# Kernel optimization log

Measured on AMD Instinct MI355X. Metric: run time of the kernel, lower is better.

Reference implementation:

```python
import jax, jax.numpy as jnp
import numpy as np
import math

DIM = 1024
NUM_HEADS = 16
HEAD_DIM = 64
NUM_FEATURES = 128
B, N = 2, 1024


def _sample_orf(rng, num_features, head_dim):
    # Orthogonal Random Features: stack QR-orthogonalized blocks scaled by chi(D) row norms
    blocks = []
    while len(blocks) * head_dim < num_features:
        G = rng.standard_normal((head_dim, head_dim)).astype(np.float32)
        Q, _ = np.linalg.qr(G)
        norms = np.linalg.norm(rng.standard_normal((head_dim, head_dim)).astype(np.float32), axis=1)
        blocks.append(np.diag(norms) @ Q.T)
    return np.concatenate(blocks, axis=0)[:num_features]


def setup_inputs() -> dict:
    key = jax.random.key(0)
    ks = jax.random.split(key, 6)
    s = 1.0 / math.sqrt(DIM)
    x = jax.random.normal(ks[0], (B, N, DIM), dtype=jnp.float32)
    omega = jnp.asarray(_sample_orf(np.random.default_rng(0), NUM_FEATURES, HEAD_DIM))
    Wq = jax.random.normal(ks[1], (DIM, DIM), dtype=jnp.float32) * s
    Wk = jax.random.normal(ks[2], (DIM, DIM), dtype=jnp.float32) * s
    Wv = jax.random.normal(ks[3], (DIM, DIM), dtype=jnp.float32) * s
    Wo = jax.random.normal(ks[4], (DIM, DIM), dtype=jnp.float32) * s
    bo = jax.random.normal(ks[5], (DIM,), dtype=jnp.float32) * 0.01
    return {"x": x, "omega": omega, "Wq": Wq, "Wk": Wk, "Wv": Wv, "Wo": Wo, "bo": bo}


def _phi(x, omega, is_query):
    # x: [B,H,N,D], omega: [M,D] -> [B,H,N,M]
    proj = jnp.einsum('bhnd,md->bhnm', x, omega)
    norm = 0.5 * jnp.sum(x * x, axis=-1, keepdims=True)
    log_phi = proj - norm
    if is_query:
        log_phi = log_phi - jnp.max(log_phi, axis=-1, keepdims=True)
    else:
        log_phi = log_phi - jnp.max(log_phi)
    return jnp.exp(log_phi) / math.sqrt(NUM_FEATURES) + 1e-4


def reference(x, omega, Wq, Wk, Wv, Wo, bo):
    Bx, Nx, _ = x.shape
    H, D = NUM_HEADS, HEAD_DIM

    def split_heads(y):  # [B,N,H*D] -> [B,H,N,D]
        return y.reshape(Bx, Nx, H, D).transpose(0, 2, 1, 3)

    q = split_heads(x @ Wq.T)
    k = split_heads(x @ Wk.T)
    v = split_heads(x @ Wv.T)

    scale = D ** (-0.25)
    phi_q = _phi(q * scale, omega, is_query=True)   # [B,H,N,M]
    phi_k = _phi(k * scale, omega, is_query=False)  # [B,H,N,M]

    # causal linear attention via explicit kv outer-product cumsum (as in source)
    kv = jnp.einsum('bhnm,bhnd->bhnmd', phi_k, v)
    kv_cumsum = jnp.cumsum(kv, axis=2)              # [B,H,N,M,D]
    k_cumsum = jnp.cumsum(phi_k, axis=2)            # [B,H,N,M]
    out = jnp.einsum('bhnm,bhnmd->bhnd', phi_q, kv_cumsum)
    z = 1.0 / (jnp.einsum('bhnm,bhnm->bhn', phi_q, k_cumsum) + 1e-6)
    out = out * z[..., None]

    out = out.transpose(0, 2, 1, 3).reshape(Bx, Nx, H * D)
    return out @ Wo.T + bo
```

## Files before the change

### kernel.cpp

```cpp
#include <hip/hip_runtime.h>
#include <hip/hip_bf16.h>
#include <math.h>

#define DIMS 1024
#define NHEADS 16
#define HDIM 64
#define NFEAT 128
#define BB 2
#define NN 1024
#define BN (BB*NN)
#define NCH 16
#define CSZ 64
#define WW (DIMS*DIMS)
#define QKVN (3*DIMS)

#define SCALE 0.3535533905932738f
#define INV_SQRT_M 0.08838834764831845f

typedef __attribute__((ext_vector_type(8))) _Float16 h8v;
typedef __attribute__((ext_vector_type(8))) short s8v;
typedef __attribute__((ext_vector_type(4))) float f4v;

__device__ __forceinline__ ushort f2h(float x) {
    _Float16 h = (_Float16)x;
    return *(ushort*)&h;
}
__device__ __forceinline__ float h2f(ushort u) {
    _Float16 h = *(_Float16*)&u;
    return (float)h;
}
__device__ __forceinline__ void gload16(const void* g, void* l) {
    __builtin_amdgcn_global_load_lds(
        (const __attribute__((address_space(1))) unsigned int*)g,
        (__attribute__((address_space(3))) unsigned int*)l,
        16, 0, 0);
}

#define NX (BN*DIMS/8)
#define NW (WW/8)
#define NOM (NFEAT*HDIM/8)
__global__ __launch_bounds__(256) void cast_all(const float* __restrict__ x,
                                                const float* __restrict__ Wq,
                                                const float* __restrict__ Wk,
                                                const float* __restrict__ Wv,
                                                const float* __restrict__ Wo,
                                                const float* __restrict__ omega,
                                                ushort* __restrict__ xh,
                                                ushort* __restrict__ wqkvh,
                                                ushort* __restrict__ woh,
                                                ushort* __restrict__ omh) {
    const int i = blockIdx.x * 256 + threadIdx.x;
    const float* src; ushort* dst; int off;
    if (i < NX)               { src = x;     dst = xh;                     off = i; }
    else if (i < NX + NW)     { src = Wq;    dst = wqkvh;                  off = i - NX; }
    else if (i < NX + 2 * NW) { src = Wk;    dst = wqkvh + WW;             off = i - NX - NW; }
    else if (i < NX + 3 * NW) { src = Wv;    dst = wqkvh + 2 * (size_t)WW; off = i - NX - 2 * NW; }
    else if (i < NX + 4 * NW) { src = Wo;    dst = woh;                    off = i - NX - 3 * NW; }
    else                      { src = omega; dst = omh;                    off = i - NX - 4 * NW; }
    float4 a = ((const float4*)src)[2 * (size_t)off];
    float4 b = ((const float4*)src)[2 * (size_t)off + 1];
    float v[8] = {a.x, a.y, a.z, a.w, b.x, b.y, b.z, b.w};
    ushort h8[8];
    #pragma unroll
    for (int j = 0; j < 8; ++j) h8[j] = f2h(v[j]);
    *(s8v*)&dst[(size_t)off * 8] = *(s8v*)&h8[0];
}

template<int BM, bool HOUT>
__global__ __launch_bounds__(256) void gemm_nt_lds(const ushort* __restrict__ A,
                                                   const ushort* __restrict__ B,
                                                   float* __restrict__ C,
                                                   ushort* __restrict__ C16,
                                                   const float* __restrict__ bias,
                                                   int M, int N, int K, int nbx) {
    constexpr int MF = BM / 32;
    constexpr int AI = BM / 32;
    __shared__ __attribute__((aligned(16))) ushort lA[BM][64];
    __shared__ __attribute__((aligned(16))) ushort lB[128][64];
    const int tid = threadIdx.x;
    const int w = tid >> 6, l = tid & 63, lr = l & 15, lg = l >> 4;
    const int wm = (w >> 1) * (BM / 2), wn = (w & 1) * 64;
    const int nwg = gridDim.x;
    const int q8 = nwg >> 3;
    const int neu = (blockIdx.x & 7) * q8 + (blockIdx.x >> 3);
    const int bx = neu % nbx, by = neu / nbx;
    const int bi = bx * BM, bj = by * 128;
    const int srow = l >> 3;
    const int scol = ((l & 7) ^ (l >> 3)) * 8;

    f4v acc[MF][4] = {};
    for (int k0 = 0; k0 < K; k0 += 64) {
        #pragma unroll
        for (int i = 0; i < AI; ++i) {
            const int r0 = w * (8 * AI) + i * 8;
            gload16(&A[(size_t)(bi + r0 + srow) * K + k0 + scol], &lA[r0][0]);
        }
        #pragma unroll
        for (int i = 0; i < 4; ++i) {
            const int r0 = w * 32 + i * 8;
            gload16(&B[(size_t)(bj + r0 + srow) * K + k0 + scol], &lB[r0][0]);
        }
        __syncthreads();
        #pragma unroll
        for (int kk = 0; kk < 2; ++kk) {
            const int soff = ((kk * 4 + lg) ^ (lr & 7)) * 8;
            h8v b_[4];
            #pragma unroll
            for (int j = 0; j < 4; ++j) b_[j] = *(h8v*)&lB[wn + j * 16 + lr][soff];
            #pragma unroll
            for (int i = 0; i < MF; ++i) {
                h8v a_ = *(h8v*)&lA[wm + i * 16 + lr][soff];
                #pragma unroll
                for (int j = 0; j < 4; ++j)
                    acc[i][j] = __builtin_amdgcn_mfma_f32_16x16x32_f16(a_, b_[j], acc[i][j], 0, 0, 0);
            }
        }
        __syncthreads();
    }
    #pragma unroll
    for (int i = 0; i < MF; ++i)
        #pragma unroll
        for (int j = 0; j < 4; ++j)
            #pragma unroll
            for (int rg = 0; rg < 4; ++rg) {
                const int row = bi + wm + i * 16 + lg * 4 + rg;
                const int col = bj + wn + j * 16 + lr;
                if (HOUT) {
                    C16[(size_t)row * N + col] = f2h(acc[i][j][rg]);
                } else {
                    float r = acc[i][j][rg] + bias[col];
                    C[(size_t)row * N + col] = r;
                }
            }
}

__global__ __launch_bounds__(256) void phi_mfma(const ushort* __restrict__ qkvh,
                                                const ushort* __restrict__ omh,
                                                ushort* __restrict__ phiq,
                                                ushort* __restrict__ plocal,
                                                float* __restrict__ blockmax,
                                                ushort* __restrict__ vt,
                                                ushort* __restrict__ ssum16,
                                                float* __restrict__ kcsum,
                                                float* __restrict__ vsum) {
    __shared__ __attribute__((aligned(16))) ushort lq[64][72];
    __shared__ __attribute__((aligned(16))) ushort lom[128 * 72];
    __shared__ __attribute__((aligned(16))) ushort lktT[128][72];
    __shared__ __attribute__((aligned(16))) ushort lv[64][72];
    __shared__ __attribute__((aligned(16))) ushort lvt[64][72];
    __shared__ float lnorm[64];
    __shared__ float wred[4];
    const int tid = threadIdx.x;
    const int z = blockIdx.z, h = blockIdx.y;
    const int bn0 = blockIdx.x * 64;
    const int w = tid >> 6, l = tid & 63, lr = l & 15, lg = l >> 4;
    const int b = blockIdx.x >> 4, c = blockIdx.x & 15;
    const int bh = b * NHEADS + h;

    {
        const int r = tid >> 2, c0 = (tid & 3) * 16;
        const size_t g = (size_t)(bn0 + r) * QKVN + (size_t)z * DIMS + h * HDIM + c0;
        s8v v0 = *(const s8v*)&qkvh[g];
        s8v v1 = *(const s8v*)&qkvh[g + 8];
        *(s8v*)&lq[r][c0] = v0;
        *(s8v*)&lq[r][c0 + 8] = v1;
        float p = 0.f;
        #pragma unroll
        for (int j = 0; j < 8; ++j) {
            float a = h2f(((ushort*)&v0)[j]); p += a * a;
            float bb2 = h2f(((ushort*)&v1)[j]); p += bb2 * bb2;
        }
        p += __shfl_xor(p, 1); p += __shfl_xor(p, 2);
        if ((tid & 3) == 0) lnorm[r] = p;
    }
    {
        const int m = tid >> 1, c0 = (tid & 1) * 32;
        #pragma unroll
        for (int i = 0; i < 4; ++i)
            *(s8v*)&lom[m * 72 + c0 + i * 8] = *(const s8v*)&omh[m * HDIM + c0 + i * 8];
    }
    if (z == 1) {
        const int r = tid >> 2, c0 = (tid & 3) * 16;
        const size_t g = (size_t)(bn0 + r) * QKVN + 2 * DIMS + h * HDIM + c0;
        *(s8v*)&lv[r][c0]     = *(const s8v*)&qkvh[g];
        *(s8v*)&lv[r][c0 + 8] = *(const s8v*)&qkvh[g + 8];
    }
    __syncthreads();

    f4v acc[8] = {};
    #pragma unroll
    for (int k0 = 0; k0 < 64; k0 += 32) {
        h8v a = *(h8v*)&lq[w * 16 + lr][k0 + lg * 8];
        #pragma unroll
        for (int ct = 0; ct < 8; ++ct) {
            h8v bo = *(h8v*)&lom[(ct * 16 + lr) * 72 + k0 + lg * 8];
            acc[ct] = __builtin_amdgcn_mfma_f32_16x16x32_f16(a, bo, acc[ct], 0, 0, 0);
        }
    }

    const float hs2 = 0.5f * SCALE * SCALE;
    float lvv[4][8];
    #pragma unroll
    for (int rg = 0; rg < 4; ++rg) {
        const int row = w * 16 + lg * 4 + rg;
        const float nh = hs2 * lnorm[row];
        #pragma unroll
        for (int ct = 0; ct < 8; ++ct) lvv[rg][ct] = SCALE * acc[ct][rg] - nh;
    }
    if (z == 1) {
        float bmax = -3.4e38f;
        #pragma unroll
        for (int rg = 0; rg < 4; ++rg)
            #pragma unroll
            for (int ct = 0; ct < 8; ++ct) bmax = fmaxf(bmax, lvv[rg][ct]);
        #pragma unroll
        for (int o = 32; o >= 1; o >>= 1) bmax = fmaxf(bmax, __shfl_xor(bmax, o));
        if (l == 0) wred[w] = bmax;
    }
    __syncthreads();

    if (z == 0) {
        #pragma unroll
        for (int rg = 0; rg < 4; ++rg) {
            const int row = w * 16 + lg * 4 + rg;
            float mx = -3.4e38f;
            #pragma unroll
            for (int ct = 0; ct < 8; ++ct) mx = fmaxf(mx, lvv[rg][ct]);
            #pragma unroll
            for (int o = 8; o >= 1; o >>= 1) mx = fmaxf(mx, __shfl_xor(mx, o));
            #pragma unroll
            for (int ct = 0; ct < 8; ++ct)
                lom[row * 136 + ct * 16 + lr] = f2h(expf(lvv[rg][ct] - mx) * INV_SQRT_M + 1e-4f);
        }
    } else {
        const float bm = fmaxf(fmaxf(wred[0], wred[1]), fmaxf(wred[2], wred[3]));
        if (tid == 0) blockmax[h * 32 + blockIdx.x] = bm;
        #pragma unroll
        for (int rg = 0; rg < 4; ++rg) {
            const int row = w * 16 + lg * 4 + rg;
            #pragma unroll
            for (int ct = 0; ct < 8; ++ct)
                lom[row * 136 + ct * 16 + lr] = f2h(expf(lvv[rg][ct] - bm));
        }
    }
    __syncthreads();

    {
        ushort* dst = (z == 0) ? phiq : plocal;
        const int r = tid >> 2, c0 = (tid & 3) * 32;
        const int br = bn0 + r;
        const int bb2 = br >> 10, n = br & (NN - 1);
        const size_t og = ((size_t)(bb2 * NHEADS + h) * NN + n) * NFEAT;
        #pragma unroll
        for (int i = 0; i < 4; ++i)
            *(s8v*)&dst[og + c0 + i * 8] = *(s8v*)&lom[r * 136 + c0 + i * 8];
    }
    if (z == 0) return;

    {
        const int m = tid >> 1, nh2 = (tid & 1) * 32;
        ushort tp[32];
        #pragma unroll
        for (int i = 0; i < 32; ++i) tp[i] = lom[(nh2 + i) * 136 + m];
        #pragma unroll
        for (int i = 0; i < 4; ++i) *(s8v*)&lktT[m][nh2 + i * 8] = *(s8v*)&tp[i * 8];
    }
    {
        const int d = tid >> 2, s0 = (tid & 3) * 16;
        ushort tp[16];
        #pragma unroll
        for (int i = 0; i < 16; ++i) tp[i] = lv[s0 + i][d];
        const size_t tb = ((size_t)bh * HDIM + d) * NN + c * CSZ + s0;
        *(s8v*)&vt[tb] = *(s8v*)&tp[0];
        *(s8v*)&vt[tb + 8] = *(s8v*)&tp[8];
        *(s8v*)&lvt[d][s0] = *(s8v*)&tp[0];
        *(s8v*)&lvt[d][s0 + 8] = *(s8v*)&tp[8];
    }
    __syncthreads();

    f4v ac2[8] = {};
    #pragma unroll
    for (int k0 = 0; k0 < 64; k0 += 32) {
        h8v a = *(h8v*)&lvt[w * 16 + lr][k0 + lg * 8];
        #pragma unroll
        for (int ct = 0; ct < 8; ++ct) {
            h8v bf = *(h8v*)&lktT[ct * 16 + lr][k0 + lg * 8];
            ac2[ct] = __builtin_amdgcn_mfma_f32_16x16x32_f16(a, bf, ac2[ct], 0, 0, 0);
        }
    }
    const size_t obase = ((size_t)bh * NCH + c) * (HDIM * NFEAT);
    #pragma unroll
    for (int ct = 0; ct < 8; ++ct)
        #pragma unroll
        for (int rg = 0; rg < 4; ++rg) {
            const int d = w * 16 + lg * 4 + rg, m = ct * 16 + lr;
            ssum16[obase + (size_t)d * NFEAT + m] = f2h(ac2[ct][rg]);
        }
    if (tid < 128) {
        float s = 0.f;
        #pragma unroll 8
        for (int i = 0; i < 64; ++i) s += h2f(lktT[tid][i]);
        kcsum[((size_t)bh * NCH + c) * NFEAT + tid] = s;
    }
    if (tid < 64) {
        float s = 0.f;
        #pragma unroll 8
        for (int i = 0; i < 64; ++i) s += h2f(lvt[tid][i]);
        vsum[((size_t)bh * NCH + c) * HDIM + tid] = s;
    }
}

__global__ __launch_bounds__(256) void scan_final(const ushort* __restrict__ phiq,
                                                  const ushort* __restrict__ plocal,
                                                  const ushort* __restrict__ vt,
                                                  const ushort* __restrict__ ssum16,
                                                  const float* __restrict__ kcsum,
                                                  const float* __restrict__ vsum,
                                                  const float* __restrict__ blockmax,
                                                  ushort* __restrict__ att_h) {
    const int c = blockIdx.x, bh = blockIdx.y;
    const int b = bh >> 4, h = bh & 15;
    const int n0 = c * CSZ;
    __shared__ __attribute__((aligned(16))) ushort lq[64][136];
    __shared__ __attribute__((aligned(16))) ushort lk[64][136];
    __shared__ __attribute__((aligned(16))) ushort lvt[64][72];
    __shared__ __attribute__((aligned(16))) ushort lsp[64][136];
    __shared__ __attribute__((aligned(16))) ushort lA[64][72];
    __shared__ float kc[NFEAT];
    __shared__ float zin[64];
    __shared__ float zp[4][64];
    __shared__ float gred[4];
    const int tid = threadIdx.x;

    float mxv = fmaxf(blockmax[tid], blockmax[tid + 256]);
    #pragma unroll
    for (int o = 32; o >= 1; o >>= 1) mxv = fmaxf(mxv, __shfl_xor(mxv, o));
    if ((tid & 63) == 0) gred[tid >> 6] = mxv;
    __syncthreads();
    const float gm = fmaxf(fmaxf(gred[0], gred[1]), fmaxf(gred[2], gred[3]));
    const float fac = expf(blockmax[h * 32 + b * 16 + c] - gm) * INV_SQRT_M;

    const size_t qb = ((size_t)bh * NN + n0) * NFEAT;
    #pragma unroll
    for (int i = 0; i < 4; ++i) {
        const int idx = tid + 256 * i;
        const int r = idx >> 4, cs = (idx & 15) * 8;
        *(s8v*)&lq[r][cs] = *(const s8v*)&phiq[qb + (size_t)r * NFEAT + cs];
        s8v pv = *(const s8v*)&plocal[qb + (size_t)r * NFEAT + cs];
        ushort t[8];
        #pragma unroll
        for (int j = 0; j < 8; ++j) t[j] = f2h(h2f(((ushort*)&pv)[j]) * fac + 1e-4f);
        *(s8v*)&lk[r][cs] = *(s8v*)&t[0];
    }
    {
        const int d = tid >> 2;
        const int m0 = (tid & 3) * 32;
        float acc[32] = {};
        float vs_tot = 0.f;
        for (int cp = 0; cp < c; ++cp) {
            const float facp = expf(blockmax[h * 32 + b * 16 + cp] - gm) * INV_SQRT_M;
            vs_tot += vsum[((size_t)bh * NCH + cp) * HDIM + d];
            const size_t cb = ((size_t)bh * NCH + cp) * (HDIM * NFEAT) + (size_t)d * NFEAT + m0;
            #pragma unroll
            for (int i = 0; i < 4; ++i) {
                s8v v = *(const s8v*)&ssum16[cb + i * 8];
                #pragma unroll
                for (int j = 0; j < 8; ++j) acc[i * 8 + j] += facp * h2f(((ushort*)&v)[j]);
            }
        }
        const float vadd = 1e-4f * vs_tot;
        ushort o[32];
        #pragma unroll
        for (int i = 0; i < 32; ++i) o[i] = f2h(acc[i] + vadd);
        #pragma unroll
        for (int i = 0; i < 4; ++i) *(s8v*)&lsp[d][m0 + i * 8] = *(s8v*)&o[i * 8];
    }
    if (tid < NFEAT) {
        float a = 0.f;
        for (int cp = 0; cp < c; ++cp) {
            const float facp = expf(blockmax[h * 32 + b * 16 + cp] - gm) * INV_SQRT_M;
            a += facp * kcsum[((size_t)bh * NCH + cp) * NFEAT + tid] + 64.0f * 1e-4f;
        }
        kc[tid] = a;
    }
    {
        const int d = tid >> 2, s = (tid & 3) * 16;
        const size_t g = ((size_t)bh * HDIM + d) * NN + n0 + s;
        *(s8v*)&lvt[d][s]     = *(const s8v*)&vt[g];
        *(s8v*)&lvt[d][s + 8] = *(const s8v*)&vt[g + 8];
    }
    __syncthreads();

    const int w = tid >> 6, l = tid & 63, lr = l & 15, lg = l >> 4;

    f4v a4[4] = {};
    #pragma unroll
    for (int k0 = 0; k0 < 128; k0 += 32) {
        h8v av = *(h8v*)&lq[w * 16 + lr][k0 + lg * 8];
        #pragma unroll
        for (int ct = 0; ct < 4; ++ct) {
            h8v bv = *(h8v*)&lk[ct * 16 + lr][k0 + lg * 8];
            a4[ct] = __builtin_amdgcn_mfma_f32_16x16x32_f16(av, bv, a4[ct], 0, 0, 0);
        }
    }
    float zi[4] = {0.f, 0.f, 0.f, 0.f};
    #pragma unroll
    for (int ct = 0; ct < 4; ++ct) {
        #pragma unroll
        for (int rg = 0; rg < 4; ++rg) {
            const int row = w * 16 + lg * 4 + rg;
            const int col = ct * 16 + lr;
            const float val = (col <= row) ? a4[ct][rg] : 0.f;
            const ushort hq = f2h(val);
            zi[rg] += h2f(hq);
            lA[row][col] = hq;
        }
    }
    #pragma unroll
    for (int rg = 0; rg < 4; ++rg) {
        float z = zi[rg];
        z += __shfl_xor(z, 1); z += __shfl_xor(z, 2);
        z += __shfl_xor(z, 4); z += __shfl_xor(z, 8);
        if (lr == 0) zin[w * 16 + lg * 4 + rg] = z;
    }
    {
        const int row = tid & 63, qq = tid >> 6;
        float s = 0.f;
        #pragma unroll 8
        for (int m = 0; m < 32; ++m) s += h2f(lq[row][qq * 32 + m]) * kc[qq * 32 + m];
        zp[qq][row] = s;
    }
    __syncthreads();

    f4v o4[4] = {};
    #pragma unroll
    for (int k0 = 0; k0 < 64; k0 += 32) {
        h8v av = *(h8v*)&lA[w * 16 + lr][k0 + lg * 8];
        #pragma unroll
        for (int ct = 0; ct < 4; ++ct) {
            h8v bv = *(h8v*)&lvt[ct * 16 + lr][k0 + lg * 8];
            o4[ct] = __builtin_amdgcn_mfma_f32_16x16x32_f16(av, bv, o4[ct], 0, 0, 0);
        }
    }
    #pragma unroll
    for (int k0 = 0; k0 < 128; k0 += 32) {
        h8v av = *(h8v*)&lq[w * 16 + lr][k0 + lg * 8];
        #pragma unroll
        for (int ct = 0; ct < 4; ++ct) {
            h8v bv = *(h8v*)&lsp[ct * 16 + lr][k0 + lg * 8];
            o4[ct] = __builtin_amdgcn_mfma_f32_16x16x32_f16(av, bv, o4[ct], 0, 0, 0);
        }
    }
    #pragma unroll
    for (int rg = 0; rg < 4; ++rg) {
        const int row = w * 16 + lg * 4 + rg;
        const float z = zin[row] + zp[0][row] + zp[1][row] + zp[2][row] + zp[3][row] + 1e-6f;
        const float rz = 1.f / z;
        #pragma unroll
        for (int ct = 0; ct < 4; ++ct) {
            const int d = ct * 16 + lr;
            att_h[((size_t)(b * NN + n0 + row)) * DIMS + h * HDIM + d] = f2h(o4[ct][rg] * rz);
        }
    }
}

extern "C" void kernel_launch(void* const* d_in, const int* in_sizes, int n_in,
                              void* d_out, int out_size, void* d_ws, size_t ws_size,
                              hipStream_t stream) {
    const float* x     = (const float*)d_in[0];
    const float* omega = (const float*)d_in[1];
    const float* Wq    = (const float*)d_in[2];
    const float* Wk    = (const float*)d_in[3];
    const float* Wv    = (const float*)d_in[4];
    const float* Wo    = (const float*)d_in[5];
    const float* bo    = (const float*)d_in[6];
    float* out = (float*)d_out;

    const size_t PROJ = (size_t)BN * DIMS;
    const size_t PHI  = (size_t)BB * NHEADS * NN * NFEAT;
    ushort* qkvh    = (ushort*)d_ws;
    ushort* xh      = qkvh + (size_t)BN * QKVN;
    ushort* wqkvh   = xh + PROJ;
    ushort* woh     = wqkvh + (size_t)QKVN * DIMS;
    ushort* omh     = woh + WW;
    ushort* phiq_h  = omh + NFEAT * HDIM;
    ushort* plocal  = phiq_h + PHI;
    ushort* vt_h    = plocal + PHI;
    ushort* ssum16  = vt_h + PROJ;
    ushort* att_hb  = ssum16 + PHI;
    float*  kcsum   = (float*)(att_hb + PROJ);
    float*  blockmax= kcsum + 32 * NCH * NFEAT;
    float*  vsum    = blockmax + 512;

    cast_all<<<(NX + 4 * NW + NOM) / 256, 256, 0, stream>>>(x, Wq, Wk, Wv, Wo, omega,
                                                            xh, wqkvh, woh, omh);

    gemm_nt_lds<64, true><<<(BN / 64) * (QKVN / 128), 256, 0, stream>>>(
        xh, wqkvh, nullptr, qkvh, nullptr, BN, QKVN, DIMS, BN / 64);

    dim3 pg(BN / 64, NHEADS, 2);
    phi_mfma<<<pg, 256, 0, stream>>>(qkvh, omh, phiq_h, plocal, blockmax,
                                     vt_h, ssum16, kcsum, vsum);

    dim3 cg(NCH, BB * NHEADS);
    scan_final<<<cg, 256, 0, stream>>>(phiq_h, plocal, vt_h, ssum16, kcsum, vsum,
                                       blockmax, att_hb);

    gemm_nt_lds<64, false><<<(BN / 64) * (DIMS / 128), 256, 0, stream>>>(
        att_hb, woh, out, nullptr, bo, BN, DIMS, DIMS, BN / 64);
}
```

Measured before the change: 86.26 us.

## Recompute phi features inside scan kernel instead of materializing phi_q and phi_k

The phi kernel no longer computes or stores phi_q and the local phi_k tensors. It now only produces the key-side block max, the transposed V, and the per-chunk summaries. The scan kernel recomputes phi_q and phi_k from the fp16 q/k projections and omega with MFMA, using a shared-memory pool that aliases buffers across phases. This removes the 2x fp16 [B,H,N,M] write and read round trip and halves the phi grid, at the cost of repeated feature-projection MFMAs and extra barriers in the scan kernel. The output projection GEMM tile height also drops from 64 to 32 rows, which doubles its block count.

```diff
diff --git a/kernel.cpp b/kernel.cpp
--- a/kernel.cpp
+++ b/kernel.cpp
@@ -134,15 +134,13 @@
             }
 }
 
-__global__ __launch_bounds__(256) void phi_mfma(const ushort* __restrict__ qkvh,
-                                                const ushort* __restrict__ omh,
-                                                ushort* __restrict__ phiq,
-                                                ushort* __restrict__ plocal,
-                                                float* __restrict__ blockmax,
-                                                ushort* __restrict__ vt,
-                                                ushort* __restrict__ ssum16,
-                                                float* __restrict__ kcsum,
-                                                float* __restrict__ vsum) {
+__global__ __launch_bounds__(256) void phik_stats(const ushort* __restrict__ qkvh,
+                                                  const ushort* __restrict__ omh,
+                                                  float* __restrict__ blockmax,
+                                                  ushort* __restrict__ vt,
+                                                  ushort* __restrict__ ssum16,
+                                                  float* __restrict__ kcsum,
+                                                  float* __restrict__ vsum) {
     __shared__ __attribute__((aligned(16))) ushort lq[64][72];
     __shared__ __attribute__((aligned(16))) ushort lom[128 * 72];
     __shared__ __attribute__((aligned(16))) ushort lktT[128][72];
@@ -151,7 +149,7 @@
     __shared__ float lnorm[64];
     __shared__ float wred[4];
     const int tid = threadIdx.x;
-    const int z = blockIdx.z, h = blockIdx.y;
+    const int h = blockIdx.y;
     const int bn0 = blockIdx.x * 64;
     const int w = tid >> 6, l = tid & 63, lr = l & 15, lg = l >> 4;
     const int b = blockIdx.x >> 4, c = blockIdx.x & 15;
@@ -159,7 +157,7 @@
 
     {
         const int r = tid >> 2, c0 = (tid & 3) * 16;
-        const size_t g = (size_t)(bn0 + r) * QKVN + (size_t)z * DIMS + h * HDIM + c0;
+        const size_t g = (size_t)(bn0 + r) * QKVN + DIMS + h * HDIM + c0;
         s8v v0 = *(const s8v*)&qkvh[g];
         s8v v1 = *(const s8v*)&qkvh[g + 8];
         *(s8v*)&lq[r][c0] = v0;
@@ -179,7 +177,7 @@
         for (int i = 0; i < 4; ++i)
             *(s8v*)&lom[m * 72 + c0 + i * 8] = *(const s8v*)&omh[m * HDIM + c0 + i * 8];
     }
-    if (z == 1) {
+    {
         const int r = tid >> 2, c0 = (tid & 3) * 16;
         const size_t g = (size_t)(bn0 + r) * QKVN + 2 * DIMS + h * HDIM + c0;
         *(s8v*)&lv[r][c0]     = *(const s8v*)&qkvh[g];
@@ -200,62 +198,32 @@
 
     const float hs2 = 0.5f * SCALE * SCALE;
     float lvv[4][8];
+    float bmax = -3.4e38f;
     #pragma unroll
     for (int rg = 0; rg < 4; ++rg) {
         const int row = w * 16 + lg * 4 + rg;
         const float nh = hs2 * lnorm[row];
         #pragma unroll
-        for (int ct = 0; ct < 8; ++ct) lvv[rg][ct] = SCALE * acc[ct][rg] - nh;
-    }
-    if (z == 1) {
-        float bmax = -3.4e38f;
-        #pragma unroll
-        for (int rg = 0; rg < 4; ++rg)
-            #pragma unroll
-            for (int ct = 0; ct < 8; ++ct) bmax = fmaxf(bmax, lvv[rg][ct]);
-        #pragma unroll
-        for (int o = 32; o >= 1; o >>= 1) bmax = fmaxf(bmax, __shfl_xor(bmax, o));
-        if (l == 0) wred[w] = bmax;
-    }
-    __syncthreads();
-
-    if (z == 0) {
-        #pragma unroll
-        for (int rg = 0; rg < 4; ++rg) {
-            const int row = w * 16 + lg * 4 + rg;
-            float mx = -3.4e38f;
-            #pragma unroll
-            for (int ct = 0; ct < 8; ++ct) mx = fmaxf(mx, lvv[rg][ct]);
-            #pragma unroll
-            for (int o = 8; o >= 1; o >>= 1) mx = fmaxf(mx, __shfl_xor(mx, o));
-            #pragma unroll
-            for (int ct = 0; ct < 8; ++ct)
-                lom[row * 136 + ct * 16 + lr] = f2h(expf(lvv[rg][ct] - mx) * INV_SQRT_M + 1e-4f);
-        }
-    } else {
-        const float bm = fmaxf(fmaxf(wred[0], wred[1]), fmaxf(wred[2], wred[3]));
-        if (tid == 0) blockmax[h * 32 + blockIdx.x] = bm;
-        #pragma unroll
-        for (int rg = 0; rg < 4; ++rg) {
-            const int row = w * 16 + lg * 4 + rg;
-            #pragma unroll
-            for (int ct = 0; ct < 8; ++ct)
-                lom[row * 136 + ct * 16 + lr] = f2h(expf(lvv[rg][ct] - bm));
-        }
-    }
-    __syncthreads();
-
-    {
-        ushort* dst = (z == 0) ? phiq : plocal;
-        const int r = tid >> 2, c0 = (tid & 3) * 32;
-        const int br = bn0 + r;
-        const int bb2 = br >> 10, n = br & (NN - 1);
-        const size_t og = ((size_t)(bb2 * NHEADS + h) * NN + n) * NFEAT;
-        #pragma unroll
-        for (int i = 0; i < 4; ++i)
-            *(s8v*)&dst[og + c0 + i * 8] = *(s8v*)&lom[r * 136 + c0 + i * 8];
-    }
-    if (z == 0) return;
+        for (int ct = 0; ct < 8; ++ct) {
+            lvv[rg][ct] = SCALE * acc[ct][rg] - nh;
+            bmax = fmaxf(bmax, lvv[rg][ct]);
+        }
+    }
+    #pragma unroll
+    for (int o = 32; o >= 1; o >>= 1) bmax = fmaxf(bmax, __shfl_xor(bmax, o));
+    if (l == 0) wred[w] = bmax;
+    __syncthreads();
+
+    const float bm = fmaxf(fmaxf(wred[0], wred[1]), fmaxf(wred[2], wred[3]));
+    if (tid == 0) blockmax[h * 32 + blockIdx.x] = bm;
+    #pragma unroll
+    for (int rg = 0; rg < 4; ++rg) {
+        const int row = w * 16 + lg * 4 + rg;
+        #pragma unroll
+        for (int ct = 0; ct < 8; ++ct)
+            lom[row * 136 + ct * 16 + lr] = f2h(expf(lvv[rg][ct] - bm));
+    }
+    __syncthreads();
 
     {
         const int m = tid >> 1, nh2 = (tid & 1) * 32;
@@ -310,48 +278,148 @@
     }
 }
 
-__global__ __launch_bounds__(256) void scan_final(const ushort* __restrict__ phiq,
-                                                  const ushort* __restrict__ plocal,
+__global__ __launch_bounds__(256) void scan_final(const ushort* __restrict__ qkvh,
+                                                  const ushort* __restrict__ omh,
                                                   const ushort* __restrict__ vt,
                                                   const ushort* __restrict__ ssum16,
                                                   const float* __restrict__ kcsum,
                                                   const float* __restrict__ vsum,
                                                   const float* __restrict__ blockmax,
                                                   ushort* __restrict__ att_h) {
-    const int c = blockIdx.x, bh = blockIdx.y;
-    const int b = bh >> 4, h = bh & 15;
-    const int n0 = c * CSZ;
-    __shared__ __attribute__((aligned(16))) ushort lq[64][136];
-    __shared__ __attribute__((aligned(16))) ushort lk[64][136];
-    __shared__ __attribute__((aligned(16))) ushort lvt[64][72];
-    __shared__ __attribute__((aligned(16))) ushort lsp[64][136];
-    __shared__ __attribute__((aligned(16))) ushort lA[64][72];
+    __shared__ __attribute__((aligned(16))) ushort pool[35840];
+    ushort (*lqt)[72]  = (ushort(*)[72]) &pool[0];
+    ushort*  lom       = &pool[4608];
+    ushort (*lvt)[72]  = (ushort(*)[72]) &pool[13824];
+    ushort (*lq)[136]  = (ushort(*)[136])&pool[18432];
+    ushort (*lk)[136]  = (ushort(*)[136])&pool[27136];
+    ushort (*lA)[72]   = (ushort(*)[72]) &pool[0];
+    ushort (*lsp)[136] = (ushort(*)[136])&pool[4608];
     __shared__ float kc[NFEAT];
     __shared__ float zin[64];
     __shared__ float zp[4][64];
     __shared__ float gred[4];
+    __shared__ float lnorm[64];
     const int tid = threadIdx.x;
-
-    float mxv = fmaxf(blockmax[tid], blockmax[tid + 256]);
-    #pragma unroll
-    for (int o = 32; o >= 1; o >>= 1) mxv = fmaxf(mxv, __shfl_xor(mxv, o));
-    if ((tid & 63) == 0) gred[tid >> 6] = mxv;
-    __syncthreads();
+    const int c = blockIdx.x, bh = blockIdx.y;
+    const int b = bh >> 4, h = bh & 15;
+    const int n0 = c * CSZ;
+    const size_t rowbase = (size_t)b * NN + n0;
+    const int w = tid >> 6, l = tid & 63, lr = l & 15, lg = l >> 4;
+
+    {
+        float mxv = fmaxf(blockmax[tid], blockmax[tid + 256]);
+        #pragma unroll
+        for (int o = 32; o >= 1; o >>= 1) mxv = fmaxf(mxv, __shfl_xor(mxv, o));
+        if (l == 0) gred[w] = mxv;
+    }
+    {
+        const int r = tid >> 2, c0 = (tid & 3) * 16;
+        const size_t g = (rowbase + r) * QKVN + h * HDIM + c0;
+        s8v v0 = *(const s8v*)&qkvh[g];
+        s8v v1 = *(const s8v*)&qkvh[g + 8];
+        *(s8v*)&lqt[r][c0] = v0;
+        *(s8v*)&lqt[r][c0 + 8] = v1;
+        float p = 0.f;
+        #pragma unroll
+        for (int j = 0; j < 8; ++j) {
+            float a = h2f(((ushort*)&v0)[j]); p += a * a;
+            float bb2 = h2f(((ushort*)&v1)[j]); p += bb2 * bb2;
+        }
+        p += __shfl_xor(p, 1); p += __shfl_xor(p, 2);
+        if ((tid & 3) == 0) lnorm[r] = p;
+    }
+    {
+        const int m = tid >> 1, c0 = (tid & 1) * 32;
+        #pragma unroll
+        for (int i = 0; i < 4; ++i)
+            *(s8v*)&lom[m * 72 + c0 + i * 8] = *(const s8v*)&omh[m * HDIM + c0 + i * 8];
+    }
+    {
+        const int d = tid >> 2, s = (tid & 3) * 16;
+        const size_t g = ((size_t)bh * HDIM + d) * NN + n0 + s;
+        *(s8v*)&lvt[d][s]     = *(const s8v*)&vt[g];
+        *(s8v*)&lvt[d][s + 8] = *(const s8v*)&vt[g + 8];
+    }
+    __syncthreads();
+
     const float gm = fmaxf(fmaxf(gred[0], gred[1]), fmaxf(gred[2], gred[3]));
-    const float fac = expf(blockmax[h * 32 + b * 16 + c] - gm) * INV_SQRT_M;
-
-    const size_t qb = ((size_t)bh * NN + n0) * NFEAT;
-    #pragma unroll
-    for (int i = 0; i < 4; ++i) {
-        const int idx = tid + 256 * i;
-        const int r = idx >> 4, cs = (idx & 15) * 8;
-        *(s8v*)&lq[r][cs] = *(const s8v*)&phiq[qb + (size_t)r * NFEAT + cs];
-        s8v pv = *(const s8v*)&plocal[qb + (size_t)r * NFEAT + cs];
-        ushort t[8];
-        #pragma unroll
-        for (int j = 0; j < 8; ++j) t[j] = f2h(h2f(((ushort*)&pv)[j]) * fac + 1e-4f);
-        *(s8v*)&lk[r][cs] = *(s8v*)&t[0];
-    }
+    const float hs2 = 0.5f * SCALE * SCALE;
+
+    {
+        f4v acc[8] = {};
+        #pragma unroll
+        for (int k0 = 0; k0 < 64; k0 += 32) {
+            h8v a = *(h8v*)&lqt[w * 16 + lr][k0 + lg * 8];
+            #pragma unroll
+            for (int ct = 0; ct < 8; ++ct) {
+                h8v bo = *(h8v*)&lom[(ct * 16 + lr) * 72 + k0 + lg * 8];
+                acc[ct] = __builtin_amdgcn_mfma_f32_16x16x32_f16(a, bo, acc[ct], 0, 0, 0);
+            }
+        }
+        #pragma unroll
+        for (int rg = 0; rg < 4; ++rg) {
+            const int row = w * 16 + lg * 4 + rg;
+            const float nh = hs2 * lnorm[row];
+            float lvv[8];
+            float mx = -3.4e38f;
+            #pragma unroll
+            for (int ct = 0; ct < 8; ++ct) {
+                lvv[ct] = SCALE * acc[ct][rg] - nh;
+                mx = fmaxf(mx, lvv[ct]);
+            }
+            #pragma unroll
+            for (int o = 8; o >= 1; o >>= 1) mx = fmaxf(mx, __shfl_xor(mx, o));
+            #pragma unroll
+            for (int ct = 0; ct < 8; ++ct)
+                lq[row][ct * 16 + lr] = f2h(expf(lvv[ct] - mx) * INV_SQRT_M + 1e-4f);
+        }
+    }
+    __syncthreads();
+
+    {
+        const int r = tid >> 2, c0 = (tid & 3) * 16;
+        const size_t g = (rowbase + r) * QKVN + DIMS + h * HDIM + c0;
+        s8v v0 = *(const s8v*)&qkvh[g];
+        s8v v1 = *(const s8v*)&qkvh[g + 8];
+        *(s8v*)&lqt[r][c0] = v0;
+        *(s8v*)&lqt[r][c0 + 8] = v1;
+        float p = 0.f;
+        #pragma unroll
+        for (int j = 0; j < 8; ++j) {
+            float a = h2f(((ushort*)&v0)[j]); p += a * a;
+            float bb2 = h2f(((ushort*)&v1)[j]); p += bb2 * bb2;
+        }
+        p += __shfl_xor(p, 1); p += __shfl_xor(p, 2);
+        if ((tid & 3) == 0) lnorm[r] = p;
+    }
+    __syncthreads();
+
+    const float bm = blockmax[h * 32 + b * 16 + c];
+    const float fac = expf(bm - gm) * INV_SQRT_M;
+    {
+        f4v acc[8] = {};
+        #pragma unroll
+        for (int k0 = 0; k0 < 64; k0 += 32) {
+            h8v a = *(h8v*)&lqt[w * 16 + lr][k0 + lg * 8];
+            #pragma unroll
+            for (int ct = 0; ct < 8; ++ct) {
+                h8v bo = *(h8v*)&lom[(ct * 16 + lr) * 72 + k0 + lg * 8];
+                acc[ct] = __builtin_amdgcn_mfma_f32_16x16x32_f16(a, bo, acc[ct], 0, 0, 0);
+            }
+        }
+        #pragma unroll
+        for (int rg = 0; rg < 4; ++rg) {
+            const int row = w * 16 + lg * 4 + rg;
+            const float nh = hs2 * lnorm[row];
+            #pragma unroll
+            for (int ct = 0; ct < 8; ++ct) {
+                const float lv = SCALE * acc[ct][rg] - nh;
+                lk[row][ct * 16 + lr] = f2h(expf(lv - bm) * fac + 1e-4f);
+            }
+        }
+    }
+    __syncthreads();
+
     {
         const int d = tid >> 2;
         const int m0 = (tid & 3) * 32;
@@ -383,15 +451,7 @@
         }
         kc[tid] = a;
     }
-    {
-        const int d = tid >> 2, s = (tid & 3) * 16;
-        const size_t g = ((size_t)bh * HDIM + d) * NN + n0 + s;
-        *(s8v*)&lvt[d][s]     = *(const s8v*)&vt[g];
-        *(s8v*)&lvt[d][s + 8] = *(const s8v*)&vt[g + 8];
-    }
-    __syncthreads();
-
-    const int w = tid >> 6, l = tid & 63, lr = l & 15, lg = l >> 4;
+    __syncthreads();
 
     f4v a4[4] = {};
     #pragma unroll
@@ -459,7 +519,7 @@
         #pragma unroll
         for (int ct = 0; ct < 4; ++ct) {
             const int d = ct * 16 + lr;
-            att_h[((size_t)(b * NN + n0 + row)) * DIMS + h * HDIM + d] = f2h(o4[ct][rg] * rz);
+            att_h[(rowbase + row) * DIMS + h * HDIM + d] = f2h(o4[ct][rg] * rz);
         }
     }
 }
@@ -483,9 +543,7 @@
     ushort* wqkvh   = xh + PROJ;
     ushort* woh     = wqkvh + (size_t)QKVN * DIMS;
     ushort* omh     = woh + WW;
-    ushort* phiq_h  = omh + NFEAT * HDIM;
-    ushort* plocal  = phiq_h + PHI;
-    ushort* vt_h    = plocal + PHI;
+    ushort* vt_h    = omh + NFEAT * HDIM;
     ushort* ssum16  = vt_h + PROJ;
     ushort* att_hb  = ssum16 + PHI;
     float*  kcsum   = (float*)(att_hb + PROJ);
@@ -498,14 +556,13 @@
     gemm_nt_lds<64, true><<<(BN / 64) * (QKVN / 128), 256, 0, stream>>>(
         xh, wqkvh, nullptr, qkvh, nullptr, BN, QKVN, DIMS, BN / 64);
 
-    dim3 pg(BN / 64, NHEADS, 2);
-    phi_mfma<<<pg, 256, 0, stream>>>(qkvh, omh, phiq_h, plocal, blockmax,
-                                     vt_h, ssum16, kcsum, vsum);
+    dim3 pg(32, NHEADS);
+    phik_stats<<<pg, 256, 0, stream>>>(qkvh, omh, blockmax, vt_h, ssum16, kcsum, vsum);
 
     dim3 cg(NCH, BB * NHEADS);
-    scan_final<<<cg, 256, 0, stream>>>(phiq_h, plocal, vt_h, ssum16, kcsum, vsum,
+    scan_final<<<cg, 256, 0, stream>>>(qkvh, omh, vt_h, ssum16, kcsum, vsum,
                                        blockmax, att_hb);
 
-    gemm_nt_lds<64, false><<<(BN / 64) * (DIMS / 128), 256, 0, stream>>>(
-        att_hb, woh, out, nullptr, bo, BN, DIMS, DIMS, BN / 64);
-}
+    gemm_nt_lds<32, false><<<(BN / 32) * (DIMS / 128), 256, 0, stream>>>(
+        att_hb, woh, out, nullptr, bo, BN, DIMS, DIMS, BN / 32);
+}
```

Result: faster. 80.31 us (-6.9%).
